# Kernel tuning notes

Hardware: AMD Instinct MI355X
Metric: run time of the kernel (lower is better)

## Reference

```python
import jax, jax.numpy as jnp
import numpy as np
import math

B, T, D = 4, 2048, 1024
H, DH = 16, 64  # n_heads, d_head; H*DH == D


def setup_inputs() -> dict:
    key = jax.random.key(0)
    ks = jax.random.split(key, 5)
    s = 0.02
    return {
        "x": jax.random.normal(ks[0], (B, T, D), dtype=jnp.float32),
        "W_qkv": jax.random.normal(ks[1], (D, 3 * D), dtype=jnp.float32) * s,
        "b_qkv": jnp.zeros((3 * D,), dtype=jnp.float32),
        "W_out": jax.random.normal(ks[2], (D, D), dtype=jnp.float32) * s,
        "b_out": jnp.zeros((D,), dtype=jnp.float32),
    }


def reference(x, W_qkv, b_qkv, W_out, b_out):
    Bx, Tx, Cx = x.shape
    qkv = x @ W_qkv + b_qkv                      # [B,T,3D]
    q, k, v = jnp.split(qkv, 3, axis=-1)
    q = q.reshape(Bx, Tx, H, DH).transpose(0, 2, 1, 3)  # [B,H,T,dh]
    k = k.reshape(Bx, Tx, H, DH).transpose(0, 2, 1, 3)
    v = v.reshape(Bx, Tx, H, DH).transpose(0, 2, 1, 3)
    scores = jnp.einsum("bhqd,bhkd->bhqk", q, k) / math.sqrt(DH)
    causal = jnp.tril(jnp.ones((Tx, Tx), dtype=bool))
    scores = jnp.where(causal, scores, jnp.float32(-jnp.inf))
    attn = jax.nn.softmax(scores, axis=-1)       # dropout p=0.0 -> identity
    out = jnp.einsum("bhqk,bhkd->bhqd", attn, v)
    out = out.transpose(0, 2, 1, 3).reshape(Bx, Tx, Cx)
    return out @ W_out + b_out
```

## Files before the change

### kernel.cpp

```cpp
#include <hip/hip_runtime.h>

#define DEVI __device__ __forceinline__

typedef __attribute__((ext_vector_type(8))) short short8;
typedef __attribute__((ext_vector_type(4))) float floatx4;

typedef const __attribute__((address_space(1))) void* gbl_ptr_t;
typedef __attribute__((address_space(3))) void* lds_ptr_t;

DEVI unsigned short f2bf(float f) {
  union { float f; unsigned int u; } v; v.f = f;
  unsigned int r = v.u + 0x7fffu + ((v.u >> 16) & 1u);
  return (unsigned short)(r >> 16);
}

DEVI float redsum16(float v) {
  v += __shfl_xor(v, 1);
  v += __shfl_xor(v, 2);
  v += __shfl_xor(v, 4);
  v += __shfl_xor(v, 8);
  return v;
}

constexpr int Bc = 4, Tc = 2048, Dc = 1024, Hc = 16, DHc = 64;
constexpr int Mrows = Bc * Tc;
constexpr long PLANE = (long)Bc * Hc * Tc * DHc;

__global__ __launch_bounds__(256) void cast_f32_bf16(const float* __restrict__ in,
                                                     unsigned short* __restrict__ out, int n4) {
  int i = blockIdx.x * 256 + threadIdx.x;
  if (i < n4) {
    float4 v = ((const float4*)in)[i];
    ushort4 o;
    o.x = f2bf(v.x); o.y = f2bf(v.y); o.z = f2bf(v.z); o.w = f2bf(v.w);
    ((ushort4*)out)[i] = o;
  }
}

__global__ __launch_bounds__(256) void transpose_cast(const float* __restrict__ in,
                                                      unsigned short* __restrict__ out,
                                                      int K, int N) {
  __shared__ float tile[32][33];
  int bx = blockIdx.x * 32;
  int by = blockIdx.y * 32;
  int tx = threadIdx.x & 31, ty = threadIdx.x >> 5;
#pragma unroll
  for (int i = ty; i < 32; i += 8) tile[i][tx] = in[(long)(by + i) * N + bx + tx];
  __syncthreads();
#pragma unroll
  for (int i = ty; i < 32; i += 8) out[(long)(bx + i) * K + by + tx] = f2bf(tile[tx][i]);
}

template <int MODE>
__global__ __launch_bounds__(256) void gemm_bt(const unsigned short* __restrict__ A,
                                               const unsigned short* __restrict__ Bt,
                                               const float* __restrict__ bias,
                                               void* __restrict__ Cout,
                                               int M, int N, int K) {
  constexpr int BK = 64;
  __shared__ __align__(16) short As[128 * 64];
  __shared__ __align__(16) short Bs[128 * 64];

  const int tid = threadIdx.x;
  const int wave = tid >> 6;
  const int lane = tid & 63;
  const int l16 = lane & 15;
  const int quad = lane >> 4;
  const int wm = (wave >> 1) * 64;
  const int wn = (wave & 1) * 64;
  const int rsub = lane >> 3;
  const int csub = (lane & 7) * 8;

  const long row0 = (long)blockIdx.y * 128;
  const long col0 = (long)blockIdx.x * 128;

  floatx4 acc[4][4];
#pragma unroll
  for (int i = 0; i < 4; i++)
#pragma unroll
    for (int j = 0; j < 4; j++) acc[i][j] = (floatx4){0.f, 0.f, 0.f, 0.f};

  for (int k0 = 0; k0 < K; k0 += BK) {
#pragma unroll
    for (int c = 0; c < 4; c++) {
      int rb = (c * 4 + wave) * 8;
      const unsigned short* sA = &A[(row0 + rb + rsub) * (long)K + k0 + csub];
      __builtin_amdgcn_global_load_lds((gbl_ptr_t)sA, (lds_ptr_t)&As[rb * 64], 16, 0, 0);
      const unsigned short* sB = &Bt[(col0 + rb + rsub) * (long)K + k0 + csub];
      __builtin_amdgcn_global_load_lds((gbl_ptr_t)sB, (lds_ptr_t)&Bs[rb * 64], 16, 0, 0);
    }
    __syncthreads();
#pragma unroll
    for (int kk = 0; kk < BK; kk += 32) {
      short8 af[4], bfr[4];
#pragma unroll
      for (int mt = 0; mt < 4; mt++)
        af[mt] = *(const short8*)&As[(wm + mt * 16 + l16) * 64 + kk + quad * 8];
#pragma unroll
      for (int nt = 0; nt < 4; nt++)
        bfr[nt] = *(const short8*)&Bs[(wn + nt * 16 + l16) * 64 + kk + quad * 8];
#pragma unroll
      for (int mt = 0; mt < 4; mt++)
#pragma unroll
        for (int nt = 0; nt < 4; nt++)
          acc[mt][nt] = __builtin_amdgcn_mfma_f32_16x16x32_bf16(af[mt], bfr[nt], acc[mt][nt], 0, 0, 0);
    }
    __syncthreads();
  }

#pragma unroll
  for (int mt = 0; mt < 4; mt++)
#pragma unroll
    for (int nt = 0; nt < 4; nt++)
#pragma unroll
      for (int r = 0; r < 4; r++) {
        long row = row0 + wm + mt * 16 + quad * 4 + r;
        long col = col0 + wn + nt * 16 + l16;
        float v = acc[mt][nt][r] + bias[col];
        if (MODE == 0) {
          int which = (int)(col >> 10);
          int hc = (int)col & 1023;
          int h = hc >> 6, d = hc & 63;
          int b = (int)(row >> 11), t = (int)row & 2047;
          ((unsigned short*)Cout)[(long)which * PLANE +
                                  (((long)(b * Hc + h) * Tc + t) << 6) + d] = f2bf(v);
        } else {
          ((float*)Cout)[row * N + col] = v;
        }
      }
}

__global__ __launch_bounds__(256) void flash_attn(const unsigned short* __restrict__ qkv,
                                                  unsigned short* __restrict__ attn_out) {
  constexpr int PD = 72;
  __shared__ __align__(16) short Ks[64 * PD];
  __shared__ __align__(16) short Vts[64 * PD];
  __shared__ __align__(16) short Ps[4 * 16 * PD];

  const int tid = threadIdx.x;
  const int wave = tid >> 6;
  const int lane = tid & 63;
  const int l16 = lane & 15;
  const int quad = lane >> 4;

  const int bh = blockIdx.y;
  const long base = (long)bh * Tc * DHc;
  const unsigned short* Qg = qkv + base;
  const unsigned short* Kg = qkv + PLANE + base;
  const unsigned short* Vg = qkv + 2 * PLANE + base;
  const int b = bh >> 4, h = bh & 15;

  constexpr float CEXP = 0.125f * 1.44269504f;
  short* Pw = &Ps[wave * 16 * PD];

  const int kr = tid >> 3;
  const int kc = (tid & 7) * 8;

#pragma unroll 1
  for (int pass = 0; pass < 2; pass++) {
    const int qx = (pass == 0) ? (int)blockIdx.x : (31 - (int)blockIdx.x);
    const int q0 = qx * 64 + wave * 16;

    short8 qf[2];
#pragma unroll
    for (int kk = 0; kk < 2; kk++)
      qf[kk] = *(const short8*)&Qg[(long)(q0 + l16) * 64 + kk * 32 + quad * 8];

    floatx4 oacc[4];
#pragma unroll
    for (int j = 0; j < 4; j++) oacc[j] = (floatx4){0.f, 0.f, 0.f, 0.f};
    float lpart[4] = {0.f, 0.f, 0.f, 0.f};

    const int ntiles = qx + 1;

    uint4 Kreg[2], Vreg[2];
    Kreg[0] = *(const uint4*)&Kg[(long)kr * 64 + kc];
    Kreg[1] = *(const uint4*)&Kg[(long)(32 + kr) * 64 + kc];
    Vreg[0] = *(const uint4*)&Vg[(long)lane * 64 + wave * 8];
    Vreg[1] = *(const uint4*)&Vg[(long)lane * 64 + (wave + 4) * 8];

#pragma unroll 1
    for (int kt = 0; kt < ntiles; kt++) {
      __syncthreads();
      *(uint4*)&Ks[kr * PD + kc] = Kreg[0];
      *(uint4*)&Ks[(32 + kr) * PD + kc] = Kreg[1];
#pragma unroll
      for (int c = 0; c < 2; c++) {
        int dc = wave + 4 * c;
        unsigned short vb[8];
        *(uint4*)vb = Vreg[c];
#pragma unroll
        for (int j = 0; j < 8; j++) Vts[(dc * 8 + j) * PD + lane] = (short)vb[j];
      }
      __syncthreads();
      if (kt + 1 < ntiles) {
        long koff = (long)(kt + 1) * 64;
        Kreg[0] = *(const uint4*)&Kg[(koff + kr) * 64 + kc];
        Kreg[1] = *(const uint4*)&Kg[(koff + 32 + kr) * 64 + kc];
        Vreg[0] = *(const uint4*)&Vg[(koff + lane) * 64 + wave * 8];
        Vreg[1] = *(const uint4*)&Vg[(koff + lane) * 64 + (wave + 4) * 8];
      }

      floatx4 sacc[4];
#pragma unroll
      for (int j = 0; j < 4; j++) sacc[j] = (floatx4){0.f, 0.f, 0.f, 0.f};
#pragma unroll
      for (int kk = 0; kk < 2; kk++) {
        short8 kf[4];
#pragma unroll
        for (int nt = 0; nt < 4; nt++)
          kf[nt] = *(const short8*)&Ks[(nt * 16 + l16) * PD + kk * 32 + quad * 8];
#pragma unroll
        for (int nt = 0; nt < 4; nt++)
          sacc[nt] = __builtin_amdgcn_mfma_f32_16x16x32_bf16(qf[kk], kf[nt], sacc[nt], 0, 0, 0);
      }

      if (kt == qx) {
#pragma unroll
        for (int nt = 0; nt < 4; nt++) {
          int ki = kt * 64 + nt * 16 + l16;
#pragma unroll
          for (int r = 0; r < 4; r++) {
            int qi = q0 + quad * 4 + r;
            if (ki > qi) sacc[nt][r] = -3.0e38f;
          }
        }
      }

#pragma unroll
      for (int nt = 0; nt < 4; nt++)
#pragma unroll
        for (int r = 0; r < 4; r++) sacc[nt][r] = exp2f(sacc[nt][r] * CEXP);
#pragma unroll
      for (int r = 0; r < 4; r++)
        lpart[r] += (sacc[0][r] + sacc[1][r]) + (sacc[2][r] + sacc[3][r]);

#pragma unroll
      for (int nt = 0; nt < 4; nt++)
#pragma unroll
        for (int r = 0; r < 4; r++)
          Pw[(quad * 4 + r) * PD + nt * 16 + l16] = (short)f2bf(sacc[nt][r]);

#pragma unroll
      for (int kk = 0; kk < 2; kk++) {
        short8 pf = *(const short8*)&Pw[l16 * PD + kk * 32 + quad * 8];
        short8 vf[4];
#pragma unroll
        for (int dt = 0; dt < 4; dt++)
          vf[dt] = *(const short8*)&Vts[(dt * 16 + l16) * PD + kk * 32 + quad * 8];
#pragma unroll
        for (int dt = 0; dt < 4; dt++)
          oacc[dt] = __builtin_amdgcn_mfma_f32_16x16x32_bf16(pf, vf[dt], oacc[dt], 0, 0, 0);
      }
    }

#pragma unroll
    for (int r = 0; r < 4; r++) {
      float l = redsum16(lpart[r]);
      float inv = 1.0f / l;
      int t = q0 + quad * 4 + r;
#pragma unroll
      for (int dt = 0; dt < 4; dt++) {
        int d = dt * 16 + l16;
        attn_out[(((long)(b * Tc + t) * Hc + h) << 6) + d] = f2bf(oacc[dt][r] * inv);
      }
    }
  }
}

extern "C" void kernel_launch(void* const* d_in, const int* in_sizes, int n_in,
                              void* d_out, int out_size, void* d_ws, size_t ws_size,
                              hipStream_t stream) {
  const float* x = (const float*)d_in[0];
  const float* Wqkv = (const float*)d_in[1];
  const float* bqkv = (const float*)d_in[2];
  const float* Wout = (const float*)d_in[3];
  const float* bout = (const float*)d_in[4];

  char* ws = (char*)d_ws;
  unsigned short* x_bf   = (unsigned short*)ws;
  unsigned short* wqkv_t = (unsigned short*)(ws + 16777216);
  unsigned short* wout_t = (unsigned short*)(ws + 16777216 + 6291456);
  unsigned short* qkv    = (unsigned short*)(ws + 25165824);
  unsigned short* attn   = x_bf;

  cast_f32_bf16<<<dim3(Mrows * Dc / 4 / 256), dim3(256), 0, stream>>>(x, x_bf, Mrows * Dc / 4);
  transpose_cast<<<dim3(3 * Dc / 32, Dc / 32), dim3(256), 0, stream>>>(Wqkv, wqkv_t, Dc, 3 * Dc);
  transpose_cast<<<dim3(Dc / 32, Dc / 32), dim3(256), 0, stream>>>(Wout, wout_t, Dc, Dc);

  gemm_bt<0><<<dim3(3 * Dc / 128, Mrows / 128), dim3(256), 0, stream>>>(
      x_bf, wqkv_t, bqkv, qkv, Mrows, 3 * Dc, Dc);

  flash_attn<<<dim3(16, Bc * Hc), dim3(256), 0, stream>>>(qkv, attn);

  gemm_bt<1><<<dim3(Dc / 128, Mrows / 128), dim3(256), 0, stream>>>(
      attn, wout_t, bout, d_out, Mrows, Dc, Dc);
}
```

Before: 322.8 us.

## Store V transposed from QKV GEMM and compute S^T for packed P stores

```diff
diff --git a/kernel.cpp b/kernel.cpp
--- a/kernel.cpp
+++ b/kernel.cpp
@@ -14,12 +14,10 @@
   return (unsigned short)(r >> 16);
 }
 
-DEVI float redsum16(float v) {
-  v += __shfl_xor(v, 1);
-  v += __shfl_xor(v, 2);
-  v += __shfl_xor(v, 4);
-  v += __shfl_xor(v, 8);
-  return v;
+DEVI unsigned int cvt_pk_bf16(float a, float b) {
+  unsigned int r;
+  asm("v_cvt_pk_bf16_f32 %0, %1, %2" : "=v"(r) : "v"(a), "v"(b));
+  return r;
 }
 
 constexpr int Bc = 4, Tc = 2048, Dc = 1024, Hc = 16, DHc = 64;
@@ -122,8 +120,13 @@
           int hc = (int)col & 1023;
           int h = hc >> 6, d = hc & 63;
           int b = (int)(row >> 11), t = (int)row & 2047;
-          ((unsigned short*)Cout)[(long)which * PLANE +
-                                  (((long)(b * Hc + h) * Tc + t) << 6) + d] = f2bf(v);
+          long addr;
+          if (which == 2) {
+            addr = 2 * PLANE + (long)((b * Hc + h) * DHc + d) * Tc + t;
+          } else {
+            addr = (long)which * PLANE + (((long)(b * Hc + h) * Tc + t) << 6) + d;
+          }
+          ((unsigned short*)Cout)[addr] = f2bf(v);
         } else {
           ((float*)Cout)[row * N + col] = v;
         }
@@ -169,36 +172,30 @@
     floatx4 oacc[4];
 #pragma unroll
     for (int j = 0; j < 4; j++) oacc[j] = (floatx4){0.f, 0.f, 0.f, 0.f};
-    float lpart[4] = {0.f, 0.f, 0.f, 0.f};
+    float lpart = 0.f;
 
     const int ntiles = qx + 1;
 
     uint4 Kreg[2], Vreg[2];
     Kreg[0] = *(const uint4*)&Kg[(long)kr * 64 + kc];
     Kreg[1] = *(const uint4*)&Kg[(long)(32 + kr) * 64 + kc];
-    Vreg[0] = *(const uint4*)&Vg[(long)lane * 64 + wave * 8];
-    Vreg[1] = *(const uint4*)&Vg[(long)lane * 64 + (wave + 4) * 8];
+    Vreg[0] = *(const uint4*)&Vg[(long)kr * Tc + kc];
+    Vreg[1] = *(const uint4*)&Vg[(long)(32 + kr) * Tc + kc];
 
 #pragma unroll 1
     for (int kt = 0; kt < ntiles; kt++) {
       __syncthreads();
       *(uint4*)&Ks[kr * PD + kc] = Kreg[0];
       *(uint4*)&Ks[(32 + kr) * PD + kc] = Kreg[1];
-#pragma unroll
-      for (int c = 0; c < 2; c++) {
-        int dc = wave + 4 * c;
-        unsigned short vb[8];
-        *(uint4*)vb = Vreg[c];
-#pragma unroll
-        for (int j = 0; j < 8; j++) Vts[(dc * 8 + j) * PD + lane] = (short)vb[j];
-      }
+      *(uint4*)&Vts[kr * PD + kc] = Vreg[0];
+      *(uint4*)&Vts[(32 + kr) * PD + kc] = Vreg[1];
       __syncthreads();
       if (kt + 1 < ntiles) {
         long koff = (long)(kt + 1) * 64;
         Kreg[0] = *(const uint4*)&Kg[(koff + kr) * 64 + kc];
         Kreg[1] = *(const uint4*)&Kg[(koff + 32 + kr) * 64 + kc];
-        Vreg[0] = *(const uint4*)&Vg[(koff + lane) * 64 + wave * 8];
-        Vreg[1] = *(const uint4*)&Vg[(koff + lane) * 64 + (wave + 4) * 8];
+        Vreg[0] = *(const uint4*)&Vg[(long)kr * Tc + koff + kc];
+        Vreg[1] = *(const uint4*)&Vg[(long)(32 + kr) * Tc + koff + kc];
       }
 
       floatx4 sacc[4];
@@ -212,34 +209,33 @@
           kf[nt] = *(const short8*)&Ks[(nt * 16 + l16) * PD + kk * 32 + quad * 8];
 #pragma unroll
         for (int nt = 0; nt < 4; nt++)
-          sacc[nt] = __builtin_amdgcn_mfma_f32_16x16x32_bf16(qf[kk], kf[nt], sacc[nt], 0, 0, 0);
+          sacc[nt] = __builtin_amdgcn_mfma_f32_16x16x32_bf16(kf[nt], qf[kk], sacc[nt], 0, 0, 0);
       }
 
       if (kt == qx) {
+        const int qi = q0 + l16;
 #pragma unroll
         for (int nt = 0; nt < 4; nt++) {
-          int ki = kt * 64 + nt * 16 + l16;
 #pragma unroll
           for (int r = 0; r < 4; r++) {
-            int qi = q0 + quad * 4 + r;
+            int ki = kt * 64 + nt * 16 + quad * 4 + r;
             if (ki > qi) sacc[nt][r] = -3.0e38f;
           }
         }
       }
 
 #pragma unroll
-      for (int nt = 0; nt < 4; nt++)
-#pragma unroll
-        for (int r = 0; r < 4; r++) sacc[nt][r] = exp2f(sacc[nt][r] * CEXP);
-#pragma unroll
-      for (int r = 0; r < 4; r++)
-        lpart[r] += (sacc[0][r] + sacc[1][r]) + (sacc[2][r] + sacc[3][r]);
-
-#pragma unroll
-      for (int nt = 0; nt < 4; nt++)
-#pragma unroll
-        for (int r = 0; r < 4; r++)
-          Pw[(quad * 4 + r) * PD + nt * 16 + l16] = (short)f2bf(sacc[nt][r]);
+      for (int nt = 0; nt < 4; nt++) {
+        float p0 = exp2f(sacc[nt][0] * CEXP);
+        float p1 = exp2f(sacc[nt][1] * CEXP);
+        float p2 = exp2f(sacc[nt][2] * CEXP);
+        float p3 = exp2f(sacc[nt][3] * CEXP);
+        lpart += (p0 + p1) + (p2 + p3);
+        uint2 w;
+        w.x = cvt_pk_bf16(p0, p1);
+        w.y = cvt_pk_bf16(p2, p3);
+        *(uint2*)&Pw[l16 * PD + nt * 16 + quad * 4] = w;
+      }
 
 #pragma unroll
       for (int kk = 0; kk < 2; kk++) {
@@ -254,10 +250,13 @@
       }
     }
 
+    float l = lpart;
+    l += __shfl_xor(l, 16);
+    l += __shfl_xor(l, 32);
 #pragma unroll
     for (int r = 0; r < 4; r++) {
-      float l = redsum16(lpart[r]);
-      float inv = 1.0f / l;
+      float lr = __shfl(l, quad * 4 + r);
+      float inv = 1.0f / lr;
       int t = q0 + quad * 4 + r;
 #pragma unroll
       for (int dt = 0; dt < 4; dt++) {
```

Measured after the change: 404.9 us. +25.4%, slower.
